# Kernel tuning notes

Hardware: AMD Instinct MI355X
Metric: run time of the kernel (lower is better)

## Reference

```python
import jax, jax.numpy as jnp
import numpy as np

B, C, H, W = 64, 3, 64, 64
F = 96          # base_filters
K = 8           # n_mixtures
h, w = H // 2, W // 2
C0 = 2 * C      # channels of each checkerboard half
SECTIONS = [C0, C0, C0 * K, C0 * K, C0 * K]
SPLITS = [int(s) for s in np.cumsum(SECTIONS)[:-1]]
EPS = 1e-6


def conv2d(x, wgt, b):
    y = jax.lax.conv_general_dilated(x, wgt, (1, 1), 'SAME',
                                     dimension_numbers=('NCHW', 'OIHW', 'NCHW'))
    return y + b[None, :, None, None]


def layer_norm(x, g, b, eps=1e-5):
    # nn.LayerNorm(mid_shape): normalize over (C,H,W) per sample
    mu = jnp.mean(x, axis=(1, 2, 3), keepdims=True)
    var = jnp.var(x, axis=(1, 2, 3), keepdims=True)
    return (x - mu) / jnp.sqrt(var + eps) * g[None] + b[None]


def checker_split(z, odd=False):
    Bz, Cz, Hz, Wz = z.shape
    z = z.reshape(Bz, Cz, Hz // 2, 2, Wz // 2, 2)
    p00 = z[:, :, :, 0, :, 0]; p01 = z[:, :, :, 0, :, 1]
    p10 = z[:, :, :, 1, :, 0]; p11 = z[:, :, :, 1, :, 1]
    z0 = jnp.concatenate([p00, p11], axis=1)  # even checkerboard
    z1 = jnp.concatenate([p01, p10], axis=1)  # odd checkerboard
    if odd:
        z0, z1 = z1, z0
    return z0, z1


def checker_merge(z0, z1, odd=False):
    if odd:
        z0, z1 = z1, z0
    Cz = z0.shape[1] // 2
    p00, p11 = z0[:, :Cz], z0[:, Cz:]
    p01, p10 = z1[:, :Cz], z1[:, Cz:]
    Bz, _, hz, wz = p00.shape
    zi = jnp.stack([jnp.stack([p00, p01], axis=-1),
                    jnp.stack([p10, p11], axis=-1)], axis=-2)  # (B,C,h,w,2i,2j)
    z = zi.transpose(0, 1, 2, 4, 3, 5).reshape(Bz, Cz, 2 * hz, 2 * wz)
    return z


def gated_attn(x, qkv_w, qkv_b, proj_w, proj_b):
    Bx, Fx, hx, wx = x.shape
    xf = x.reshape(Bx, Fx, hx * wx).transpose(0, 2, 1)  # (B, L, F)
    qkv = xf @ qkv_w.T + qkv_b
    q, k, v = jnp.split(qkv, 3, axis=-1)
    scores = jnp.einsum('bqf,bkf->bqk', q, k) / jnp.sqrt(jnp.float32(Fx))
    attn = jax.nn.softmax(scores, axis=-1)
    o = jnp.einsum('bqk,bkf->bqf', attn, v)
    g = o @ proj_w.T + proj_b
    ga, gb = jnp.split(g, 2, axis=-1)
    out = xf + ga * jax.nn.sigmoid(gb)  # gated residual
    return out.transpose(0, 2, 1).reshape(Bx, Fx, hx, wx)


def conditioner(z1, conv1_w, conv1_b, gconv_w, gconv_b, ln1_g, ln1_b,
                qkv_w, qkv_b, proj_w, proj_b, ln2_g, ln2_b, conv2_w, conv2_b):
    x = conv2d(z1, conv1_w, conv1_b)
    g = conv2d(x, gconv_w, gconv_b)
    ga, gb = jnp.split(g, 2, axis=1)
    x = x + ga * jax.nn.sigmoid(gb)          # GatedConv2d
    x = layer_norm(x, ln1_g, ln1_b)
    x = gated_attn(x, qkv_w, qkv_b, proj_w, proj_b)
    x = layer_norm(x, ln2_g, ln2_b)
    return conv2d(x, conv2_w, conv2_b)


def _forward(z, log_df_dz, conv1_w, conv1_b, gconv_w, gconv_b, ln1_g, ln1_b,
             qkv_w, qkv_b, proj_w, proj_b, ln2_g, ln2_b, conv2_w, conv2_b,
             a_log_scale, a_bias):
    z0, z1 = checker_split(z)
    params = conditioner(z1, conv1_w, conv1_b, gconv_w, gconv_b, ln1_g, ln1_b,
                         qkv_w, qkv_b, proj_w, proj_b, ln2_g, ln2_b, conv2_w, conv2_b)
    a, b, logpi, mu, s = jnp.split(params, SPLITS, axis=1)
    a = jnp.tanh(a) * a_log_scale + a_bias
    Bz = z0.shape[0]
    logpi = jax.nn.log_softmax(logpi.reshape(Bz, K, C0, h, w), axis=1)
    mu = mu.reshape(Bz, K, C0, h, w)
    s = s.reshape(Bz, K, C0, h, w)
    # mixture-of-logistics CDF
    u = (z0[:, None] - mu) * jnp.exp(-s)
    x = jnp.sum(jnp.exp(logpi) * jax.nn.sigmoid(u), axis=1)
    log_pdf = jax.scipy.special.logsumexp(
        logpi - s + jax.nn.log_sigmoid(u) + jax.nn.log_sigmoid(-u), axis=1)
    log_df_dz = log_df_dz + jnp.sum(log_pdf.reshape(Bz, -1), axis=1)
    # logit transform
    x = jnp.clip(x, EPS, 1.0 - EPS)
    z0n = jnp.log(x) - jnp.log1p(-x)
    log_df_dz = log_df_dz + jnp.sum((-jnp.log(x) - jnp.log1p(-x)).reshape(Bz, -1), axis=1)
    # affine rescale
    z0n = z0n * jnp.exp(a) + b
    log_df_dz = log_df_dz + jnp.sum(a.reshape(Bz, -1), axis=1)
    return checker_merge(z0n, z1), log_df_dz


def setup_inputs() -> dict:
    key = jax.random.key(0)
    ks = jax.random.split(key, 10)
    sc = 0.05
    return dict(
        z=jax.random.normal(ks[0], (B, C, H, W), jnp.float32),
        log_df_dz=jnp.zeros((B,), jnp.float32),
        conv1_w=sc * jax.random.normal(ks[1], (F, C0, 3, 3), jnp.float32),
        conv1_b=jnp.zeros((F,), jnp.float32),
        gconv_w=sc * jax.random.normal(ks[2], (2 * F, F, 3, 3), jnp.float32),
        gconv_b=jnp.zeros((2 * F,), jnp.float32),
        ln1_g=jnp.ones((F, h, w), jnp.float32),
        ln1_b=jnp.zeros((F, h, w), jnp.float32),
        qkv_w=sc * jax.random.normal(ks[3], (3 * F, F), jnp.float32),
        qkv_b=jnp.zeros((3 * F,), jnp.float32),
        proj_w=sc * jax.random.normal(ks[4], (2 * F, F), jnp.float32),
        proj_b=jnp.zeros((2 * F,), jnp.float32),
        ln2_g=jnp.ones((F, h, w), jnp.float32),
        ln2_b=jnp.zeros((F, h, w), jnp.float32),
        conv2_w=sc * jax.random.normal(ks[5], (sum(SECTIONS), F, 3, 3), jnp.float32),
        conv2_b=jnp.zeros((sum(SECTIONS),), jnp.float32),
        a_log_scale=0.01 * jax.random.normal(ks[6], (1,), jnp.float32),
        a_bias=0.01 * jax.random.normal(ks[7], (1,), jnp.float32),
    )


def reference(z, log_df_dz, conv1_w, conv1_b, gconv_w, gconv_b, ln1_g, ln1_b,
              qkv_w, qkv_b, proj_w, proj_b, ln2_g, ln2_b, conv2_w, conv2_b,
              a_log_scale, a_bias):
    return _forward(z, log_df_dz, conv1_w, conv1_b, gconv_w, gconv_b, ln1_g, ln1_b,
                    qkv_w, qkv_b, proj_w, proj_b, ln2_g, ln2_b, conv2_w, conv2_b,
                    a_log_scale, a_bias)
```

## Files before the change

### kernel.cpp

```cpp
#include <hip/hip_runtime.h>
#include <cstdint>
#include <cstddef>


typedef unsigned short u16;
typedef __attribute__((ext_vector_type(8))) short short8;
typedef __attribute__((ext_vector_type(4))) float f32x4;
typedef __attribute__((ext_vector_type(4))) unsigned int u32x4;

__device__ __forceinline__ float sigm(float x){ return 1.0f/(1.0f+__expf(-x)); }

__device__ __forceinline__ u16 f2bf(float f){
    unsigned int u = __float_as_uint(f);
    u += 0x7fffu + ((u >> 16) & 1u);
    return (u16)(u >> 16);
}
__device__ __forceinline__ float bf2f(u16 v){
    unsigned int u = ((unsigned int)v) << 16;
    return __uint_as_float(u);
}

__device__ __forceinline__ void dma16(const u16* g, u16* l){
    __builtin_amdgcn_global_load_lds(
        (const __attribute__((address_space(1))) void*)g,
        (__attribute__((address_space(3))) void*)l,
        16, 0, 0);
}

__device__ __forceinline__ float ex2(float x){
    float r; asm("v_exp_f32 %0, %1" : "=v"(r) : "v"(x)); return r;
}
__device__ __forceinline__ unsigned cvtpk(float lo, float hi){
    unsigned r; asm("v_cvt_pk_bf16_f32 %0, %1, %2" : "=v"(r) : "v"(lo), "v"(hi)); return r;
}
__device__ __forceinline__ void plswap32(unsigned &a, unsigned &b){
    asm("v_permlane32_swap_b32 %0, %1" : "+v"(a), "+v"(b));
}
__device__ __forceinline__ void plswap16(unsigned &a, unsigned &b){
    asm("v_permlane16_swap_b32 %0, %1" : "+v"(a), "+v"(b));
}

#define SOFTPACK(S, LACC, PA) do { \
    unsigned pk_[4][2]; \
    _Pragma("unroll") \
    for (int t=0;t<4;++t){ \
        float e0 = ex2(S[t][0]); \
        float e1 = ex2(S[t][1]); \
        float e2 = ex2(S[t][2]); \
        float e3 = ex2(S[t][3]); \
        LACC += (e0+e1)+(e2+e3); \
        pk_[t][0] = cvtpk(e0,e1); \
        pk_[t][1] = cvtpk(e2,e3); \
    } \
    _Pragma("unroll") \
    for (int kk=0;kk<2;++kk){ \
        unsigned a0 = pk_[2*kk][0], b0 = pk_[2*kk+1][0]; \
        unsigned a1 = pk_[2*kk][1], b1 = pk_[2*kk+1][1]; \
        plswap32(a0,b0); plswap16(a0,b0); \
        plswap32(a1,b1); plswap16(a1,b1); \
        u32x4 dw_; dw_[0]=a0; dw_[1]=a1; dw_[2]=b0; dw_[3]=b1; \
        PA[kk] = __builtin_bit_cast(short8, dw_); \
    } \
} while(0)

__device__ __forceinline__ short8 ln_frag(const u16* __restrict__ xg,
    const float* __restrict__ gt, const float* __restrict__ bt,
    int p, int c0, float mu, float rr)
{
    short8 x8 = *reinterpret_cast<const short8*>(xg + (size_t)p*96 + c0);
    const float* gp = gt + (size_t)p*96 + c0;
    const float* bp = bt + (size_t)p*96 + c0;
    short8 o;
    #pragma unroll
    for (int j=0;j<8;++j){
        float ag = rr*gp[j];
        o[j] = (short)f2bf(bf2f((u16)x8[j])*ag + (bp[j] - mu*ag));
    }
    return o;
}

__global__ __launch_bounds__(256) void k_prep(
    const float* __restrict__ z, const float* __restrict__ c1w, const float* __restrict__ c1b,
    const float* __restrict__ gw, const float* __restrict__ c2w,
    const float* __restrict__ qkvw, const float* __restrict__ pw,
    const float* __restrict__ ln1g, const float* __restrict__ ln1b,
    const float* __restrict__ ln2g, const float* __restrict__ ln2b,
    const float* __restrict__ logdf,
    u16* __restrict__ x1b,
    u16* __restrict__ Wg, u16* __restrict__ W2,
    u16* __restrict__ Wqkv, u16* __restrict__ Wproj,
    float* __restrict__ gt1, float* __restrict__ bt1,
    float* __restrict__ gt2, float* __restrict__ bt2,
    float* __restrict__ outlog)
{
    int blk = blockIdx.x;
    int tid = threadIdx.x;
    __shared__ float tin[6][6][34];
    __shared__ __align__(16) u16 Wc[96][72];
    __shared__ __align__(16) u16 imc[128][72];

    if (blk < 512){
        int b  = blk >> 3;
        int pg = blk & 7;
        int r0 = pg*4;
        for (int e = tid; e < 96*72; e += 256){
            int oc = e/72, k = e%72;
            Wc[oc][k] = (k < 54) ? f2bf(c1w[oc*54 + k]) : (u16)0;
        }
        for (int idx = tid; idx < 6*6*34; idx += 256){
            int c = idx/204, rem = idx%204;
            int rr = rem/34, q = rem%34;
            int ii = r0 - 1 + rr, jj = q - 1;
            float v = 0.f;
            if ((unsigned)ii < 32u && (unsigned)jj < 32u){
                if (c < 3) v = z[((b*3+c)*64 + 2*ii)*64 + (2*jj+1)];
                else       v = z[((b*3+(c-3))*64 + (2*ii+1))*64 + 2*jj];
            }
            tin[c][rr][q] = v;
        }
        __syncthreads();
        for (int e = tid; e < 128*72; e += 256){
            int px = e/72, k = e%72;
            float v = 0.f;
            if (k < 54){
                int c = k/9, rr = (k%9)/3, dcc = k%3;
                v = tin[c][(px>>5)+rr][(px&31)+dcc];
            }
            imc[px][k] = f2bf(v);
        }
        __syncthreads();

        int w = tid >> 6, lane = tid & 63;
        int cc = lane & 15, gg = lane >> 4;
        f32x4 acc[2][6];
        #pragma unroll
        for (int u=0;u<2;++u)
            #pragma unroll
            for (int t=0;t<6;++t) acc[u][t] = (f32x4){0.f,0.f,0.f,0.f};

        #pragma unroll
        for (int ks=0; ks<2; ++ks){
            short8 a0 = *reinterpret_cast<const short8*>(&imc[w*32 + cc     ][ks*32 + 8*gg]);
            short8 a1 = *reinterpret_cast<const short8*>(&imc[w*32 + 16 + cc][ks*32 + 8*gg]);
            #pragma unroll
            for (int t=0; t<6; ++t){
                short8 bb = *reinterpret_cast<const short8*>(&Wc[t*16+cc][ks*32 + 8*gg]);
                acc[0][t] = __builtin_amdgcn_mfma_f32_16x16x32_bf16(a0, bb, acc[0][t], 0,0,0);
                acc[1][t] = __builtin_amdgcn_mfma_f32_16x16x32_bf16(a1, bb, acc[1][t], 0,0,0);
            }
        }

        #pragma unroll
        for (int u=0;u<2;++u){
            int p0 = pg*128 + w*32 + u*16 + gg*4;
            #pragma unroll
            for (int t=0;t<6;++t){
                int oc = t*16+cc;
                float bv = c1b[oc];
                #pragma unroll
                for (int r=0;r<4;++r)
                    x1b[((size_t)(b*1024) + p0 + r)*96 + oc] = f2bf(acc[u][t][r] + bv);
            }
        }
    } else if (blk < 1160){
        int idx = (blk-512)*256 + tid;
        int j = idx & 7;
        int lane = (idx >> 3) & 63;
        int fo = idx >> 9;
        int frag = fo % 18;
        int tob = fo / 18;
        int obk = tob & 1, tap = tob >> 1;
        int t = frag/3, ks = frag%3;
        int cc = lane & 15, gg = lane >> 4;
        int ocp = obk*96 + t*16 + cc;
        int r2 = ocp%96, isB = r2/48, i2 = r2%48;
        int oc = (ocp/96)*48 + i2 + isB*96;
        int ic = ks*32 + 8*gg + j;
        Wg[idx] = f2bf(gw[(size_t)(oc*96+ic)*9 + tap]);
    } else if (blk < 1700){
        int idx = (blk-1160)*256 + tid;
        int j = idx & 7;
        int lane = (idx >> 3) & 63;
        int fo = idx >> 9;
        int frag = fo % 15;
        int tob = fo / 15;
        int obk = tob & 1, tap = tob >> 1;
        int t = frag/3, ks = frag%3;
        int cc = lane & 15, gg = lane >> 4;
        int oc = obk*80 + t*16 + cc;
        int ic = ks*32 + 8*gg + j;
        W2[idx] = (oc < 156) ? f2bf(c2w[(size_t)(oc*96+ic)*9 + tap]) : (u16)0;
    } else if (blk < 1808){
        int idx = (blk-1700)*256 + tid;
        int j = idx & 7;
        int lane = (idx >> 3) & 63;
        int fo = idx >> 9;
        int frag = fo % 27;
        int obk = fo / 27;
        int t = frag/3, ks = frag%3;
        int cc = lane & 15, gg = lane >> 4;
        int n = obk*144 + t*16 + cc;
        int ic = ks*32 + 8*gg + j;
        Wqkv[idx] = f2bf(qkvw[(size_t)n*96 + ic]);
    } else if (blk < 1880){
        int idx = (blk-1808)*256 + tid;
        int j = idx & 7;
        int lane = (idx >> 3) & 63;
        int fo = idx >> 9;
        int frag = fo % 18;
        int obk = fo / 18;
        int t = frag/3, ks = frag%3;
        int cc = lane & 15, gg = lane >> 4;
        int ocp = obk*96 + t*16 + cc;
        int r2 = ocp%96, isB = r2/48, i2 = r2%48;
        int oc = obk*48 + i2 + isB*96;
        int ic = ks*32 + 8*gg + j;
        Wproj[idx] = f2bf(pw[(size_t)oc*96 + ic]);
    } else if (blk < 2264){
        int idx = (blk-1880)*256 + tid;
        int c = idx >> 10, p = idx & 1023;
        gt1[p*96 + c] = ln1g[idx];
    } else if (blk < 2648){
        int idx = (blk-2264)*256 + tid;
        int c = idx >> 10, p = idx & 1023;
        bt1[p*96 + c] = ln1b[idx];
    } else if (blk < 3032){
        int idx = (blk-2648)*256 + tid;
        int c = idx >> 10, p = idx & 1023;
        gt2[p*96 + c] = ln2g[idx];
    } else if (blk < 3416){
        int idx = (blk-3032)*256 + tid;
        int c = idx >> 10, p = idx & 1023;
        bt2[p*96 + c] = ln2b[idx];
    } else {
        if (tid < 64) outlog[tid] = logdf[tid];
    }
}

__global__ __launch_bounds__(256,4) void k_gconv(const u16* __restrict__ Xpb,
    const u16* __restrict__ Wt, const float* __restrict__ bias,
    u16* __restrict__ outb, float* __restrict__ partials)
{
    int blk  = blockIdx.x;
    int obk  = blk & 1;
    int pblk = (blk >> 1) & 7;
    int b    = blk >> 4;
    int tid  = threadIdx.x;
    int w = tid >> 6, lane = tid & 63;
    int cc = lane & 15, gg = lane >> 4;

    __shared__ __align__(16) u16 Ws[2][9216];
    __shared__ float red[8];

    f32x4 acc[2][6];
    #pragma unroll
    for (int u=0;u<2;++u)
        #pragma unroll
        for (int t=0;t<6;++t) acc[u][t] = (f32x4){0.f,0.f,0.f,0.f};

    int base = pblk*128 + w*32;
    int ia = base >> 5;
    const u16* xb = Xpb + (size_t)b*1024*96;

    {
        const u16* src = Wt + (size_t)obk*9216;
        #pragma unroll
        for (int i=0;i<5;++i){
            int c = tid + 256*i;
            if (c < 1152) dma16(src + (size_t)c*8, Ws[0] + (size_t)(w*64+256*i)*8);
        }
    }

    for (int tap=0; tap<9; ++tap){
        __syncthreads();
        if (tap < 8){
            const u16* src = Wt + (size_t)((tap+1)*2 + obk)*9216;
            int nb = (tap+1)&1;
            #pragma unroll
            for (int i=0;i<5;++i){
                int c = tid + 256*i;
                if (c < 1152) dma16(src + (size_t)c*8, Ws[nb] + (size_t)(w*64+256*i)*8);
            }
        }
        const u16* Wc = Ws[tap&1];
        int dr = tap/3 - 1, dc = tap%3 - 1;

        int ii = ia + dr;
        int jj0 = cc + dc, jj1 = cc + 16 + dc;
        bool rv = ((unsigned)ii < 32u);
        bool v0 = rv && ((unsigned)jj0 < 32u);
        bool v1 = rv && ((unsigned)jj1 < 32u);
        const u16* ar0 = xb + (ptrdiff_t)(ii*32 + jj0)*96 + 8*gg;
        const u16* ar1 = xb + (ptrdiff_t)(ii*32 + jj1)*96 + 8*gg;

        #pragma unroll
        for (int ks=0; ks<3; ++ks){
            short8 a0 = {0,0,0,0,0,0,0,0};
            short8 a1 = {0,0,0,0,0,0,0,0};
            if (v0) a0 = *reinterpret_cast<const short8*>(ar0 + ks*32);
            if (v1) a1 = *reinterpret_cast<const short8*>(ar1 + ks*32);
            #pragma unroll
            for (int t=0; t<6; ++t){
                short8 bb = *reinterpret_cast<const short8*>(Wc + ((size_t)(t*3+ks)*64 + lane)*8);
                acc[0][t] = __builtin_amdgcn_mfma_f32_16x16x32_bf16(a0, bb, acc[0][t], 0,0,0);
                acc[1][t] = __builtin_amdgcn_mfma_f32_16x16x32_bf16(a1, bb, acc[1][t], 0,0,0);
            }
        }
    }

    float s = 0.f, ssq = 0.f;
    #pragma unroll
    for (int u=0;u<2;++u){
        int p0 = base + u*16 + gg*4;
        #pragma unroll
        for (int t=0;t<3;++t){
            int ocA = obk*48 + t*16+cc;
            float ba = bias[ocA], bbv = bias[ocA+96];
            #pragma unroll
            for (int r=0;r<4;++r){
                float res = bf2f(Xpb[((size_t)b*1024 + p0+r)*96 + ocA]);
                float va = acc[u][t][r]   + ba;
                float vb = acc[u][t+3][r] + bbv;
                float v = res + va*sigm(vb);
                outb[((size_t)b*1024 + p0+r)*96 + ocA] = f2bf(v);
                s += v; ssq += v*v;
            }
        }
    }
    #pragma unroll
    for (int o=32;o>0;o>>=1){ s += __shfl_down(s,o,64); ssq += __shfl_down(ssq,o,64); }
    if (lane==0){ red[w]=s; red[4+w]=ssq; }
    __syncthreads();
    if (tid==0){
        int slot = b*16 + pblk*2 + obk;
        partials[slot*2+0] = red[0]+red[1]+red[2]+red[3];
        partials[slot*2+1] = red[4]+red[5]+red[6]+red[7];
    }
}

__global__ __launch_bounds__(256) void k_lne(const u16* __restrict__ xb,
    const float* __restrict__ gt, const float* __restrict__ bt,
    const float* __restrict__ partials, u16* __restrict__ out)
{
    int b = blockIdx.x / 48, rem = blockIdx.x % 48;
    float s=0.f, ss=0.f;
    #pragma unroll
    for (int i=0;i<16;++i){ s += partials[(b*16+i)*2]; ss += partials[(b*16+i)*2+1]; }
    float mu = s/98304.f;
    float r = rsqrtf(ss/98304.f - mu*mu + 1e-5f);

    int e8 = rem*256 + threadIdx.x;
    size_t base = (size_t)b*98304 + (size_t)e8*8;
    short8 x8 = *reinterpret_cast<const short8*>(xb + base);
    const float* gp = gt + e8*8;
    const float* bp = bt + e8*8;
    short8 o8;
    #pragma unroll
    for (int i=0;i<8;++i)
        o8[i] = (short)f2bf((bf2f((u16)x8[i]) - mu)*r*gp[i] + bp[i]);
    *reinterpret_cast<short8*>(out + base) = o8;
}

__global__ __launch_bounds__(256,4) void k_conv2m(const u16* __restrict__ Xpb,
    const u16* __restrict__ Wt, const float* __restrict__ bias,
    u16* __restrict__ out)
{
    int blk  = blockIdx.x;
    int obk  = blk & 1;
    int pblk = (blk >> 1) & 7;
    int b    = blk >> 4;
    int tid  = threadIdx.x;
    int w = tid >> 6, lane = tid & 63;
    int cc = lane & 15, gg = lane >> 4;

    __shared__ __align__(16) u16 Ws[2][7680];

    f32x4 acc[2][5];
    #pragma unroll
    for (int u=0;u<2;++u)
        #pragma unroll
        for (int t=0;t<5;++t) acc[u][t] = (f32x4){0.f,0.f,0.f,0.f};

    int base = pblk*128 + w*32;
    int ia = base >> 5;
    const u16* xb = Xpb + (size_t)b*1024*96;

    {
        const u16* src = Wt + (size_t)obk*7680;
        #pragma unroll
        for (int i=0;i<4;++i){
            int c = tid + 256*i;
            if (c < 960) dma16(src + (size_t)c*8, Ws[0] + (size_t)(w*64+256*i)*8);
        }
    }

    for (int tap=0; tap<9; ++tap){
        __syncthreads();
        if (tap < 8){
            const u16* src = Wt + (size_t)((tap+1)*2 + obk)*7680;
            int nb = (tap+1)&1;
            #pragma unroll
            for (int i=0;i<4;++i){
                int c = tid + 256*i;
                if (c < 960) dma16(src + (size_t)c*8, Ws[nb] + (size_t)(w*64+256*i)*8);
            }
        }
        const u16* Wc = Ws[tap&1];
        int dr = tap/3 - 1, dc = tap%3 - 1;

        int ii = ia + dr;
        int jj0 = cc + dc, jj1 = cc + 16 + dc;
        bool rv = ((unsigned)ii < 32u);
        bool v0 = rv && ((unsigned)jj0 < 32u);
        bool v1 = rv && ((unsigned)jj1 < 32u);
        const u16* ar0 = xb + (ptrdiff_t)(ii*32 + jj0)*96 + 8*gg;
        const u16* ar1 = xb + (ptrdiff_t)(ii*32 + jj1)*96 + 8*gg;

        #pragma unroll
        for (int ks=0; ks<3; ++ks){
            short8 a0 = {0,0,0,0,0,0,0,0};
            short8 a1 = {0,0,0,0,0,0,0,0};
            if (v0) a0 = *reinterpret_cast<const short8*>(ar0 + ks*32);
            if (v1) a1 = *reinterpret_cast<const short8*>(ar1 + ks*32);
            #pragma unroll
            for (int t=0; t<5; ++t){
                short8 bb = *reinterpret_cast<const short8*>(Wc + ((size_t)(t*3+ks)*64 + lane)*8);
                acc[0][t] = __builtin_amdgcn_mfma_f32_16x16x32_bf16(a0, bb, acc[0][t], 0,0,0);
                acc[1][t] = __builtin_amdgcn_mfma_f32_16x16x32_bf16(a1, bb, acc[1][t], 0,0,0);
            }
        }
    }

    #pragma unroll
    for (int u=0;u<2;++u){
        int p0 = base + u*16 + gg*4;
        #pragma unroll
        for (int t=0;t<5;++t){
            int oc = obk*80 + t*16+cc;
            if (oc < 156){
                float bv = bias[oc];
                u16* op = out + ((size_t)b*156 + oc)*1024 + p0;
                #pragma unroll
                for (int r=0;r<4;++r) op[r] = f2bf(acc[u][t][r] + bv);
            }
        }
    }
}

__global__ __launch_bounds__(256,4) void k_qkvm(const u16* __restrict__ Xg,
    const float* __restrict__ gt, const float* __restrict__ bt,
    const float* __restrict__ part,
    const u16* __restrict__ Wt, const float* __restrict__ bias,
    u16* __restrict__ Qb, u16* __restrict__ Kf, u16* __restrict__ Vf)
{
    int blk  = blockIdx.x;
    int obk  = blk & 1;
    int pblk = (blk >> 1) & 7;
    int b    = blk >> 4;
    int tid  = threadIdx.x;
    int w = tid >> 6, lane = tid & 63;
    int cc = lane & 15, gg = lane >> 4;
    const float scale = 0.14724445f;

    __shared__ __align__(16) u16 Ws[13824];
    {
        const u16* src = Wt + (size_t)obk*13824;
        #pragma unroll
        for (int i=0;i<7;++i){
            int c = tid + 256*i;
            if (c < 1728) dma16(src + (size_t)c*8, Ws + (size_t)(w*64+256*i)*8);
        }
    }

    float sS=0.f, sQ=0.f;
    #pragma unroll
    for (int i=0;i<16;++i){ sS += part[(b*16+i)*2]; sQ += part[(b*16+i)*2+1]; }
    float mu = sS/98304.f;
    float rr = rsqrtf(sQ/98304.f - mu*mu + 1e-5f);

    f32x4 acc[2][9];
    #pragma unroll
    for (int u=0;u<2;++u)
        #pragma unroll
        for (int t=0;t<9;++t) acc[u][t] = (f32x4){0.f,0.f,0.f,0.f};

    int base = pblk*128 + w*32;
    const u16* xg = Xg + (size_t)b*1024*96;
    __syncthreads();

    #pragma unroll
    for (int ks=0; ks<3; ++ks){
        int c0 = ks*32 + 8*gg;
        short8 a0 = ln_frag(xg, gt, bt, base+cc,    c0, mu, rr);
        short8 a1 = ln_frag(xg, gt, bt, base+cc+16, c0, mu, rr);
        #pragma unroll
        for (int t=0; t<9; ++t){
            short8 bb = *reinterpret_cast<const short8*>(Ws + ((size_t)(t*3+ks)*64 + lane)*8);
            acc[0][t] = __builtin_amdgcn_mfma_f32_16x16x32_bf16(a0, bb, acc[0][t], 0,0,0);
            acc[1][t] = __builtin_amdgcn_mfma_f32_16x16x32_bf16(a1, bb, acc[1][t], 0,0,0);
        }
    }

    #pragma unroll
    for (int u=0;u<2;++u){
        int p0 = base + u*16 + gg*4;
        #pragma unroll
        for (int t=0;t<9;++t){
            int n = obk*144 + t*16+cc;
            float bv = bias[n];
            #pragma unroll
            for (int r=0;r<4;++r){
                int p = p0 + r;
                float av = acc[u][t][r] + bv;
                if (n < 96){
                    Qb[((size_t)(b*1024+p))*96 + n] = f2bf(av*scale);
                } else if (n < 192){
                    int f = n-96;
                    int jt = p>>6, t16 = (p>>4)&3, ccs = p&15;
                    int ks = f>>5, ggs = (f>>3)&3, j = f&7;
                    Kf[(size_t)(b*16+jt)*6144 + (size_t)(((t16*3+ks)*4+ggs)*16+ccs)*8 + j] = f2bf(av);
                } else {
                    int f = n-192;
                    int jt = p>>6, kl = p&63;
                    int kk = kl>>5, ggs = (kl>>3)&3, j = kl&7;
                    int ft = f>>4, ccs = f&15;
                    Vf[(size_t)(b*16+jt)*6144 + (size_t)(((ft*2+kk)*4+ggs)*16+ccs)*8 + j] = f2bf(av);
                }
            }
        }
    }
}

__global__ __launch_bounds__(256,2) void k_attn(const u16* __restrict__ Qb,
    const u16* __restrict__ Kf, const u16* __restrict__ Vf, u16* __restrict__ Ob)
{
    int qt = blockIdx.x >> 6;
    int b  = blockIdx.x & 63;
    int tid = threadIdx.x;
    int w  = tid >> 6;
    int lane = tid & 63;
    int cc = lane & 15;
    int gg = lane >> 4;

    __shared__ __align__(16) u16 Ks[3][6144];
    __shared__ __align__(16) u16 Vs[3][6144];

    int q0 = qt*128 + w*32;

    short8 qf[2][3];
    {
        const u16* qr0 = Qb + ((size_t)(b*1024 + q0 + cc))*96;
        #pragma unroll
        for (int ks=0; ks<3; ++ks){
            qf[0][ks] = *reinterpret_cast<const short8*>(qr0 + ks*32 + 8*gg);
            qf[1][ks] = *reinterpret_cast<const short8*>(qr0 + (size_t)16*96 + ks*32 + 8*gg);
        }
    }

    f32x4 Oacc[2][6];
    #pragma unroll
    for (int u=0;u<2;++u)
        #pragma unroll
        for (int ft=0; ft<6; ++ft) Oacc[u][ft] = (f32x4){0.f,0.f,0.f,0.f};
    float l_acc[2] = {0.f, 0.f};

    const u16* Kb0 = Kf + (size_t)(b*16)*6144;
    const u16* Vb0 = Vf + (size_t)(b*16)*6144;

    #pragma unroll
    for (int i=0;i<3;++i){
        size_t c8 = (size_t)(tid + 256*i)*8;
        size_t l8 = (size_t)(w*64 + 256*i)*8;
        dma16(Kb0 + c8, Ks[0] + l8);
        dma16(Vb0 + c8, Vs[0] + l8);
    }
    #pragma unroll
    for (int i=0;i<3;++i){
        size_t c8 = (size_t)(6144 + (tid + 256*i)*8);
        size_t l8 = (size_t)(w*64 + 256*i)*8;
        dma16(Kb0 + c8, Ks[1] + l8);
        dma16(Vb0 + c8, Vs[1] + l8);
    }

    for (int jt=0; jt<16; ++jt){
        if (jt < 15) asm volatile("s_waitcnt vmcnt(6)" ::: "memory");
        else         asm volatile("s_waitcnt vmcnt(0)" ::: "memory");
        __builtin_amdgcn_s_barrier();
        __builtin_amdgcn_sched_barrier(0);

        if (jt < 14){
            const u16* kn = Kb0 + (size_t)(jt+2)*6144;
            const u16* vn = Vb0 + (size_t)(jt+2)*6144;
            u16* kd = Ks[(jt+2)%3];
            u16* vd = Vs[(jt+2)%3];
            #pragma unroll
            for (int i=0;i<3;++i){
                size_t c8 = (size_t)(tid + 256*i)*8;
                size_t l8 = (size_t)(w*64 + 256*i)*8;
                dma16(kn + c8, kd + l8);
                dma16(vn + c8, vd + l8);
            }
        }

        const u16* Kc = Ks[jt%3];
        const u16* Vc = Vs[jt%3];

        f32x4 S0[4], S1[4];
        #pragma unroll
        for (int t=0;t<4;++t){ S0[t] = (f32x4){0.f,0.f,0.f,0.f}; S1[t] = (f32x4){0.f,0.f,0.f,0.f}; }

        __builtin_amdgcn_s_setprio(1);
        #pragma unroll
        for (int ks=0; ks<3; ++ks){
            #pragma unroll
            for (int t=0; t<4; ++t){
                short8 kb = *reinterpret_cast<const short8*>(Kc + ((t*3+ks)*64 + lane)*8);
                S0[t] = __builtin_amdgcn_mfma_f32_16x16x32_bf16(kb, qf[0][ks], S0[t], 0,0,0);
                S1[t] = __builtin_amdgcn_mfma_f32_16x16x32_bf16(kb, qf[1][ks], S1[t], 0,0,0);
            }
        }
        __builtin_amdgcn_s_setprio(0);

        short8 pa0[2], pa1[2];
        SOFTPACK(S0, l_acc[0], pa0);
        SOFTPACK(S1, l_acc[1], pa1);

        __builtin_amdgcn_s_setprio(1);
        #pragma unroll
        for (int kk=0; kk<2; ++kk){
            #pragma unroll
            for (int ft=0; ft<6; ++ft){
                short8 vb = *reinterpret_cast<const short8*>(Vc + ((ft*2+kk)*64 + lane)*8);
                Oacc[0][ft] = __builtin_amdgcn_mfma_f32_16x16x32_bf16(pa0[kk], vb, Oacc[0][ft], 0,0,0);
                Oacc[1][ft] = __builtin_amdgcn_mfma_f32_16x16x32_bf16(pa1[kk], vb, Oacc[1][ft], 0,0,0);
            }
        }
        __builtin_amdgcn_s_setprio(0);
    }

    #pragma unroll
    for (int u=0;u<2;++u){
        float lv = l_acc[u];
        lv += __shfl_xor(lv, 16, 64);
        lv += __shfl_xor(lv, 32, 64);
        float linv[4];
        #pragma unroll
        for (int r=0;r<4;++r) linv[r] = 1.0f / __shfl(lv, 4*gg + r, 64);
        #pragma unroll
        for (int ft=0; ft<6; ++ft)
            #pragma unroll
            for (int r=0; r<4; ++r)
                Ob[((size_t)(b*1024 + q0 + u*16 + 4*gg + r))*96 + ft*16 + cc]
                    = f2bf(Oacc[u][ft][r]*linv[r]);
    }
}

__global__ __launch_bounds__(256,4) void k_projm(const u16* __restrict__ Opb,
    const u16* __restrict__ Wt, const float* __restrict__ bias,
    const u16* __restrict__ Xg, const float* __restrict__ gt, const float* __restrict__ bt,
    const float* __restrict__ part1,
    u16* __restrict__ outb, float* __restrict__ partials)
{
    int blk  = blockIdx.x;
    int obk  = blk & 1;
    int pblk = (blk >> 1) & 7;
    int b    = blk >> 4;
    int tid  = threadIdx.x;
    int w = tid >> 6, lane = tid & 63;
    int cc = lane & 15, gg = lane >> 4;

    __shared__ __align__(16) u16 Ws[9216];
    __shared__ float red[8];
    {
        const u16* src = Wt + (size_t)obk*9216;
        #pragma unroll
        for (int i=0;i<5;++i){
            int c = tid + 256*i;
            if (c < 1152) dma16(src + (size_t)c*8, Ws + (size_t)(w*64+256*i)*8);
        }
    }

    float sS=0.f, sQ=0.f;
    #pragma unroll
    for (int i=0;i<16;++i){ sS += part1[(b*16+i)*2]; sQ += part1[(b*16+i)*2+1]; }
    float mu1 = sS/98304.f;
    float rr1 = rsqrtf(sQ/98304.f - mu1*mu1 + 1e-5f);

    f32x4 acc[2][6];
    #pragma unroll
    for (int u=0;u<2;++u)
        #pragma unroll
        for (int t=0;t<6;++t) acc[u][t] = (f32x4){0.f,0.f,0.f,0.f};

    int base = pblk*128 + w*32;
    const u16* xb = Opb + ((size_t)b*1024 + base)*96;
    __syncthreads();

    #pragma unroll
    for (int ks=0; ks<3; ++ks){
        short8 a0 = *reinterpret_cast<const short8*>(xb + (size_t)cc*96      + ks*32 + 8*gg);
        short8 a1 = *reinterpret_cast<const short8*>(xb + (size_t)(cc+16)*96 + ks*32 + 8*gg);
        #pragma unroll
        for (int t=0; t<6; ++t){
            short8 bb = *reinterpret_cast<const short8*>(Ws + ((size_t)(t*3+ks)*64 + lane)*8);
            acc[0][t] = __builtin_amdgcn_mfma_f32_16x16x32_bf16(a0, bb, acc[0][t], 0,0,0);
            acc[1][t] = __builtin_amdgcn_mfma_f32_16x16x32_bf16(a1, bb, acc[1][t], 0,0,0);
        }
    }

    const u16* resb = Xg + (size_t)b*1024*96;
    float s = 0.f, ssq = 0.f;
    #pragma unroll
    for (int u=0;u<2;++u){
        int p0 = base + u*16 + gg*4;
        #pragma unroll
        for (int t=0;t<3;++t){
            int ocA = obk*48 + t*16+cc;
            float ba = bias[ocA], bbv = bias[ocA+96];
            #pragma unroll
            for (int r=0;r<4;++r){
                int pl = p0 + r;
                float ga = acc[u][t][r]   + ba;
                float gb = acc[u][t+3][r] + bbv;
                float xv = bf2f(resb[(size_t)pl*96 + ocA]);
                float res = (xv - mu1)*rr1*gt[(size_t)pl*96 + ocA] + bt[(size_t)pl*96 + ocA];
                float v = res + ga * sigm(gb);
                outb[((size_t)b*1024 + pl)*96 + ocA] = f2bf(v);
                s += v; ssq += v*v;
            }
        }
    }
    #pragma unroll
    for (int o=32;o>0;o>>=1){ s += __shfl_down(s,o,64); ssq += __shfl_down(ssq,o,64); }
    if (lane==0){ red[w]=s; red[4+w]=ssq; }
    __syncthreads();
    if (tid==0){
        int slot = b*16 + pblk*2 + obk;
        partials[slot*2+0] = red[0]+red[1]+red[2]+red[3];
        partials[slot*2+1] = red[4]+red[5]+red[6]+red[7];
    }
}

__global__ __launch_bounds__(256) void k_mix(const float* __restrict__ z,
    const u16* __restrict__ params, const float* __restrict__ a_ls_p,
    const float* __restrict__ a_b_p, float* __restrict__ out_z, float* __restrict__ out_log)
{
    int b = blockIdx.x / 24;
    int rem = blockIdx.x % 24;
    int c0 = rem / 4;
    int pix = (rem & 3)*256 + threadIdx.x;
    int i = pix >> 5, j = pix & 31;
    float als = a_ls_p[0], abv = a_b_p[0];
    const u16* pb = params + (size_t)b*156*1024;
    float logacc = 0.f;

    if (c0 < 3){
        int idx01 = ((b*3+c0)*64 + 2*i)*64 + 2*j+1;
        int idx10 = ((b*3+c0)*64 + 2*i+1)*64 + 2*j;
        out_z[idx01] = z[idx01];
        out_z[idx10] = z[idx10];
    }

    {
        float z0v = (c0<3) ? z[((b*3+c0)*64 + 2*i)*64 + 2*j]
                           : z[((b*3+(c0-3))*64 + 2*i+1)*64 + 2*j+1];
        float a_raw = bf2f(pb[(c0)*1024 + pix]);
        float bco   = bf2f(pb[(6+c0)*1024 + pix]);
        float lp[8], mu[8], sv[8];
        float m1 = -1e30f;
        #pragma unroll
        for (int k=0;k<8;++k){
            lp[k] = bf2f(pb[(12 + k*6 + c0)*1024 + pix]);
            mu[k] = bf2f(pb[(60 + k*6 + c0)*1024 + pix]);
            sv[k] = bf2f(pb[(108 + k*6 + c0)*1024 + pix]);
            m1 = fmaxf(m1, lp[k]);
        }
        float se = 0.f;
        #pragma unroll
        for (int k=0;k<8;++k) se += __expf(lp[k]-m1);
        float lse = m1 + __logf(se);
        float xm = 0.f, mt = -1e30f;
        float t[8];
        #pragma unroll
        for (int k=0;k<8;++k){
            float lpn = lp[k] - lse;
            float u = (z0v - mu[k]) * __expf(-sv[k]);
            float au = fabsf(u);
            xm += __expf(lpn) * (1.f/(1.f+__expf(-u)));
            float lss = -(au + 2.f*log1pf(__expf(-au)));
            float tk = lpn - sv[k] + lss;
            t[k] = tk; mt = fmaxf(mt, tk);
        }
        float se2 = 0.f;
        #pragma unroll
        for (int k=0;k<8;++k) se2 += __expf(t[k]-mt);
        logacc += mt + __logf(se2);
        xm = fminf(fmaxf(xm, 1e-6f), 1.f-1e-6f);
        float lx = __logf(xm), l1x = log1pf(-xm);
        logacc += -lx - l1x;
        float aa = tanhf(a_raw)*als + abv;
        float z0n = (lx - l1x)*__expf(aa) + bco;
        logacc += aa;
        int oidx = (c0<3) ? ((b*3+c0)*64 + 2*i)*64 + 2*j
                          : ((b*3+(c0-3))*64 + 2*i+1)*64 + 2*j+1;
        out_z[oidx] = z0n;
    }

    #pragma unroll
    for (int o=32;o>0;o>>=1) logacc += __shfl_down(logacc, o, 64);
    __shared__ float part[4];
    if ((threadIdx.x&63)==0) part[threadIdx.x>>6] = logacc;
    __syncthreads();
    if (threadIdx.x==0){
        atomicAdd(out_log + b, part[0]+part[1]+part[2]+part[3]);
    }
}

extern "C" void kernel_launch(void* const* d_in, const int* in_sizes, int n_in,
                              void* d_out, int out_size, void* d_ws, size_t ws_size,
                              hipStream_t stream)
{
    const float* z     = (const float*)d_in[0];
    const float* logdf = (const float*)d_in[1];
    const float* c1w   = (const float*)d_in[2];
    const float* c1b   = (const float*)d_in[3];
    const float* gw    = (const float*)d_in[4];
    const float* gcb   = (const float*)d_in[5];
    const float* ln1g  = (const float*)d_in[6];
    const float* ln1b  = (const float*)d_in[7];
    const float* qkvw  = (const float*)d_in[8];
    const float* qkvb  = (const float*)d_in[9];
    const float* pw    = (const float*)d_in[10];
    const float* pbb   = (const float*)d_in[11];
    const float* ln2g  = (const float*)d_in[12];
    const float* ln2b  = (const float*)d_in[13];
    const float* c2w   = (const float*)d_in[14];
    const float* c2b   = (const float*)d_in[15];
    const float* als   = (const float*)d_in[16];
    const float* ab    = (const float*)d_in[17];

    float* out_z   = (float*)d_out;
    float* out_log = out_z + 786432;

    float* ws     = (float*)d_ws;
    u16*   x1b    = (u16*)(ws + 0);
    u16*   xg_b   = (u16*)(ws + 3145728);
    u16*   Kf     = (u16*)(ws + 6291456);
    u16*   Vf     = (u16*)(ws + 9437184);
    u16*   Ob     = (u16*)(ws + 12582912);
    u16*   x2b    = (u16*)(ws + 15728640);
    u16*   Qb     = x1b;
    u16*   xln2b  = Kf;
    u16*   params = (u16*)(ws + 9437184);
    const size_t T = 19660800;
    float* gt1    = ws + T;
    float* bt1    = ws + T + 98304;
    float* gt2    = ws + T + 196608;
    float* bt2    = ws + T + 294912;
    float* part1  = ws + T + 393216;
    float* part2  = ws + T + 395264;
    u16*   Wg     = (u16*)(ws + T + 397568);
    u16*   W2     = (u16*)(ws + T + 480512);
    u16*   Wqkv   = (u16*)(ws + T + 549632);
    u16*   Wproj  = (u16*)(ws + T + 563456);

    k_prep   <<<3417, 256, 0, stream>>>(z, c1w, c1b, gw, c2w, qkvw, pw,
                                        ln1g, ln1b, ln2g, ln2b, logdf,
                                        x1b, Wg, W2, Wqkv, Wproj,
                                        gt1, bt1, gt2, bt2, out_log);
    k_gconv  <<<1024, 256, 0, stream>>>(x1b, Wg, gcb, xg_b, part1);
    k_qkvm   <<<1024, 256, 0, stream>>>(xg_b, gt1, bt1, part1, Wqkv, qkvb, Qb, Kf, Vf);
    k_attn   <<<512, 256, 0, stream>>>(Qb, Kf, Vf, Ob);
    k_projm  <<<1024, 256, 0, stream>>>(Ob, Wproj, pbb, xg_b, gt1, bt1, part1, x2b, part2);
    k_lne    <<<3072, 256, 0, stream>>>(x2b, gt2, bt2, part2, xln2b);
    k_conv2m <<<1024, 256, 0, stream>>>(xln2b, W2, c2b, params);
    k_mix    <<<1536, 256, 0, stream>>>(z, params, als, ab, out_z, out_log);
}
```

Before: 269.8 us.

## Fuse conv2 and mixture-logistic coupling into one kernel via shared memory

Merges the final 3x3 conv (k_conv2m) and the mixture coupling kernel (k_mix) into one kernel. Each block now computes all 156 output channels for its 128-pixel tile, stages the bf16 params in LDS and runs the mixture math directly from LDS. This removes the global write and read of the params tensor and one launch. In exchange each block does twice the MFMA work with twice as many accumulators, uses about 60KB of LDS, and launches only 512 blocks at an occupancy bound of 2, which lowers parallelism.

```diff
diff --git a/kernel.cpp b/kernel.cpp
--- a/kernel.cpp
+++ b/kernel.cpp
@@ -361,92 +361,6 @@
     *reinterpret_cast<short8*>(out + base) = o8;
 }
 
-__global__ __launch_bounds__(256,4) void k_conv2m(const u16* __restrict__ Xpb,
-    const u16* __restrict__ Wt, const float* __restrict__ bias,
-    u16* __restrict__ out)
-{
-    int blk  = blockIdx.x;
-    int obk  = blk & 1;
-    int pblk = (blk >> 1) & 7;
-    int b    = blk >> 4;
-    int tid  = threadIdx.x;
-    int w = tid >> 6, lane = tid & 63;
-    int cc = lane & 15, gg = lane >> 4;
-
-    __shared__ __align__(16) u16 Ws[2][7680];
-
-    f32x4 acc[2][5];
-    #pragma unroll
-    for (int u=0;u<2;++u)
-        #pragma unroll
-        for (int t=0;t<5;++t) acc[u][t] = (f32x4){0.f,0.f,0.f,0.f};
-
-    int base = pblk*128 + w*32;
-    int ia = base >> 5;
-    const u16* xb = Xpb + (size_t)b*1024*96;
-
-    {
-        const u16* src = Wt + (size_t)obk*7680;
-        #pragma unroll
-        for (int i=0;i<4;++i){
-            int c = tid + 256*i;
-            if (c < 960) dma16(src + (size_t)c*8, Ws[0] + (size_t)(w*64+256*i)*8);
-        }
-    }
-
-    for (int tap=0; tap<9; ++tap){
-        __syncthreads();
-        if (tap < 8){
-            const u16* src = Wt + (size_t)((tap+1)*2 + obk)*7680;
-            int nb = (tap+1)&1;
-            #pragma unroll
-            for (int i=0;i<4;++i){
-                int c = tid + 256*i;
-                if (c < 960) dma16(src + (size_t)c*8, Ws[nb] + (size_t)(w*64+256*i)*8);
-            }
-        }
-        const u16* Wc = Ws[tap&1];
-        int dr = tap/3 - 1, dc = tap%3 - 1;
-
-        int ii = ia + dr;
-        int jj0 = cc + dc, jj1 = cc + 16 + dc;
-        bool rv = ((unsigned)ii < 32u);
-        bool v0 = rv && ((unsigned)jj0 < 32u);
-        bool v1 = rv && ((unsigned)jj1 < 32u);
-        const u16* ar0 = xb + (ptrdiff_t)(ii*32 + jj0)*96 + 8*gg;
-        const u16* ar1 = xb + (ptrdiff_t)(ii*32 + jj1)*96 + 8*gg;
-
-        #pragma unroll
-        for (int ks=0; ks<3; ++ks){
-            short8 a0 = {0,0,0,0,0,0,0,0};
-            short8 a1 = {0,0,0,0,0,0,0,0};
-            if (v0) a0 = *reinterpret_cast<const short8*>(ar0 + ks*32);
-            if (v1) a1 = *reinterpret_cast<const short8*>(ar1 + ks*32);
-            #pragma unroll
-            for (int t=0; t<5; ++t){
-                short8 bb = *reinterpret_cast<const short8*>(Wc + ((size_t)(t*3+ks)*64 + lane)*8);
-                acc[0][t] = __builtin_amdgcn_mfma_f32_16x16x32_bf16(a0, bb, acc[0][t], 0,0,0);
-                acc[1][t] = __builtin_amdgcn_mfma_f32_16x16x32_bf16(a1, bb, acc[1][t], 0,0,0);
-            }
-        }
-    }
-
-    #pragma unroll
-    for (int u=0;u<2;++u){
-        int p0 = base + u*16 + gg*4;
-        #pragma unroll
-        for (int t=0;t<5;++t){
-            int oc = obk*80 + t*16+cc;
-            if (oc < 156){
-                float bv = bias[oc];
-                u16* op = out + ((size_t)b*156 + oc)*1024 + p0;
-                #pragma unroll
-                for (int r=0;r<4;++r) op[r] = f2bf(acc[u][t][r] + bv);
-            }
-        }
-    }
-}
-
 __global__ __launch_bounds__(256,4) void k_qkvm(const u16* __restrict__ Xg,
     const float* __restrict__ gt, const float* __restrict__ bt,
     const float* __restrict__ part,
@@ -741,60 +655,143 @@
     }
 }
 
-__global__ __launch_bounds__(256) void k_mix(const float* __restrict__ z,
-    const u16* __restrict__ params, const float* __restrict__ a_ls_p,
+__global__ __launch_bounds__(256,2) void k_c2mix(const u16* __restrict__ Xpb,
+    const u16* __restrict__ Wt, const float* __restrict__ bias,
+    const float* __restrict__ z, const float* __restrict__ a_ls_p,
     const float* __restrict__ a_b_p, float* __restrict__ out_z, float* __restrict__ out_log)
 {
-    int b = blockIdx.x / 24;
-    int rem = blockIdx.x % 24;
-    int c0 = rem / 4;
-    int pix = (rem & 3)*256 + threadIdx.x;
-    int i = pix >> 5, j = pix & 31;
+    int blk  = blockIdx.x;
+    int pblk = blk & 7;
+    int b    = blk >> 3;
+    int tid  = threadIdx.x;
+    int w = tid >> 6, lane = tid & 63;
+    int cc = lane & 15, gg = lane >> 4;
+
+    __shared__ __align__(16) u16 SM[30720];
+    __shared__ float red[4];
+
+    f32x4 acc[2][10];
+    #pragma unroll
+    for (int u=0;u<2;++u)
+        #pragma unroll
+        for (int t=0;t<10;++t) acc[u][t] = (f32x4){0.f,0.f,0.f,0.f};
+
+    int base = pblk*128 + w*32;
+    int ia = base >> 5;
+    const u16* xb = Xpb + (size_t)b*1024*96;
+
+    {
+        #pragma unroll
+        for (int i=0;i<8;++i){
+            int c = tid + 256*i;
+            if (c < 1920) dma16(Wt + (size_t)c*8, SM + (size_t)(w*64+256*i)*8);
+        }
+    }
+
+    for (int tap=0; tap<9; ++tap){
+        __syncthreads();
+        if (tap < 8){
+            const u16* src = Wt + (size_t)(tap+1)*15360;
+            u16* dst = SM + (size_t)((tap+1)&1)*15360;
+            #pragma unroll
+            for (int i=0;i<8;++i){
+                int c = tid + 256*i;
+                if (c < 1920) dma16(src + (size_t)c*8, dst + (size_t)(w*64+256*i)*8);
+            }
+        }
+        const u16* Wc = SM + (size_t)(tap&1)*15360;
+        int dr = tap/3 - 1, dc = tap%3 - 1;
+
+        int ii = ia + dr;
+        int jj0 = cc + dc, jj1 = cc + 16 + dc;
+        bool rv = ((unsigned)ii < 32u);
+        bool v0 = rv && ((unsigned)jj0 < 32u);
+        bool v1 = rv && ((unsigned)jj1 < 32u);
+        const u16* ar0 = xb + (ptrdiff_t)(ii*32 + jj0)*96 + 8*gg;
+        const u16* ar1 = xb + (ptrdiff_t)(ii*32 + jj1)*96 + 8*gg;
+
+        #pragma unroll
+        for (int ks=0; ks<3; ++ks){
+            short8 a0 = {0,0,0,0,0,0,0,0};
+            short8 a1 = {0,0,0,0,0,0,0,0};
+            if (v0) a0 = *reinterpret_cast<const short8*>(ar0 + ks*32);
+            if (v1) a1 = *reinterpret_cast<const short8*>(ar1 + ks*32);
+            #pragma unroll
+            for (int t=0; t<10; ++t){
+                int fl = (t<5) ? (t*3+ks) : (15 + (t-5)*3 + ks);
+                short8 bb = *reinterpret_cast<const short8*>(Wc + ((size_t)fl*64 + lane)*8);
+                acc[0][t] = __builtin_amdgcn_mfma_f32_16x16x32_bf16(a0, bb, acc[0][t], 0,0,0);
+                acc[1][t] = __builtin_amdgcn_mfma_f32_16x16x32_bf16(a1, bb, acc[1][t], 0,0,0);
+            }
+        }
+    }
+
+    __syncthreads();
+    #pragma unroll
+    for (int u=0;u<2;++u){
+        int lp0 = w*32 + u*16 + gg*4;
+        #pragma unroll
+        for (int t=0;t<10;++t){
+            int oc = (t<5) ? (t*16+cc) : (80 + (t-5)*16 + cc);
+            if (oc < 156){
+                float bv = bias[oc];
+                #pragma unroll
+                for (int r=0;r<4;++r)
+                    SM[oc*132 + lp0 + r] = f2bf(acc[u][t][r] + bv);
+            }
+        }
+    }
+    __syncthreads();
+
     float als = a_ls_p[0], abv = a_b_p[0];
-    const u16* pb = params + (size_t)b*156*1024;
-    float logacc = 0.f;
-
-    if (c0 < 3){
-        int idx01 = ((b*3+c0)*64 + 2*i)*64 + 2*j+1;
-        int idx10 = ((b*3+c0)*64 + 2*i+1)*64 + 2*j;
-        out_z[idx01] = z[idx01];
-        out_z[idx10] = z[idx10];
-    }
-
-    {
+    float logsum = 0.f;
+    #pragma unroll
+    for (int e3=0;e3<3;++e3){
+        int e  = tid + 256*e3;
+        int c0 = e >> 7, xp = e & 127;
+        int pix = pblk*128 + xp;
+        int i = pix >> 5, j = pix & 31;
+
+        if (c0 < 3){
+            int idx01 = ((b*3+c0)*64 + 2*i)*64 + 2*j+1;
+            int idx10 = ((b*3+c0)*64 + 2*i+1)*64 + 2*j;
+            out_z[idx01] = z[idx01];
+            out_z[idx10] = z[idx10];
+        }
+
         float z0v = (c0<3) ? z[((b*3+c0)*64 + 2*i)*64 + 2*j]
                            : z[((b*3+(c0-3))*64 + 2*i+1)*64 + 2*j+1];
-        float a_raw = bf2f(pb[(c0)*1024 + pix]);
-        float bco   = bf2f(pb[(6+c0)*1024 + pix]);
-        float lp[8], mu[8], sv[8];
+        float a_raw = bf2f(SM[(c0)*132 + xp]);
+        float bco   = bf2f(SM[(6+c0)*132 + xp]);
+        float lpk[8], muk[8], svk[8];
         float m1 = -1e30f;
         #pragma unroll
         for (int k=0;k<8;++k){
-            lp[k] = bf2f(pb[(12 + k*6 + c0)*1024 + pix]);
-            mu[k] = bf2f(pb[(60 + k*6 + c0)*1024 + pix]);
-            sv[k] = bf2f(pb[(108 + k*6 + c0)*1024 + pix]);
-            m1 = fmaxf(m1, lp[k]);
+            lpk[k] = bf2f(SM[(12 + k*6 + c0)*132 + xp]);
+            muk[k] = bf2f(SM[(60 + k*6 + c0)*132 + xp]);
+            svk[k] = bf2f(SM[(108 + k*6 + c0)*132 + xp]);
+            m1 = fmaxf(m1, lpk[k]);
         }
         float se = 0.f;
         #pragma unroll
-        for (int k=0;k<8;++k) se += __expf(lp[k]-m1);
+        for (int k=0;k<8;++k) se += __expf(lpk[k]-m1);
         float lse = m1 + __logf(se);
         float xm = 0.f, mt = -1e30f;
-        float t[8];
+        float tk[8];
         #pragma unroll
         for (int k=0;k<8;++k){
-            float lpn = lp[k] - lse;
-            float u = (z0v - mu[k]) * __expf(-sv[k]);
+            float lpn = lpk[k] - lse;
+            float u = (z0v - muk[k]) * __expf(-svk[k]);
             float au = fabsf(u);
             xm += __expf(lpn) * (1.f/(1.f+__expf(-u)));
             float lss = -(au + 2.f*log1pf(__expf(-au)));
-            float tk = lpn - sv[k] + lss;
-            t[k] = tk; mt = fmaxf(mt, tk);
+            float t2 = lpn - svk[k] + lss;
+            tk[k] = t2; mt = fmaxf(mt, t2);
         }
         float se2 = 0.f;
         #pragma unroll
-        for (int k=0;k<8;++k) se2 += __expf(t[k]-mt);
-        logacc += mt + __logf(se2);
+        for (int k=0;k<8;++k) se2 += __expf(tk[k]-mt);
+        float logacc = mt + __logf(se2);
         xm = fminf(fmaxf(xm, 1e-6f), 1.f-1e-6f);
         float lx = __logf(xm), l1x = log1pf(-xm);
         logacc += -lx - l1x;
@@ -804,16 +801,14 @@
         int oidx = (c0<3) ? ((b*3+c0)*64 + 2*i)*64 + 2*j
                           : ((b*3+(c0-3))*64 + 2*i+1)*64 + 2*j+1;
         out_z[oidx] = z0n;
-    }
-
-    #pragma unroll
-    for (int o=32;o>0;o>>=1) logacc += __shfl_down(logacc, o, 64);
-    __shared__ float part[4];
-    if ((threadIdx.x&63)==0) part[threadIdx.x>>6] = logacc;
+        logsum += logacc;
+    }
+
+    #pragma unroll
+    for (int o=32;o>0;o>>=1) logsum += __shfl_down(logsum, o, 64);
+    if (lane==0) red[w] = logsum;
     __syncthreads();
-    if (threadIdx.x==0){
-        atomicAdd(out_log + b, part[0]+part[1]+part[2]+part[3]);
-    }
+    if (tid==0) atomicAdd(out_log + b, red[0]+red[1]+red[2]+red[3]);
 }
 
 extern "C" void kernel_launch(void* const* d_in, const int* in_sizes, int n_in,
@@ -851,7 +846,6 @@
     u16*   x2b    = (u16*)(ws + 15728640);
     u16*   Qb     = x1b;
     u16*   xln2b  = Kf;
-    u16*   params = (u16*)(ws + 9437184);
     const size_t T = 19660800;
     float* gt1    = ws + T;
     float* bt1    = ws + T + 98304;
@@ -873,6 +867,5 @@
     k_attn   <<<512, 256, 0, stream>>>(Qb, Kf, Vf, Ob);
     k_projm  <<<1024, 256, 0, stream>>>(Ob, Wproj, pbb, xg_b, gt1, bt1, part1, x2b, part2);
     k_lne    <<<3072, 256, 0, stream>>>(x2b, gt2, bt2, part2, xln2b);
-    k_conv2m <<<1024, 256, 0, stream>>>(xln2b, W2, c2b, params);
-    k_mix    <<<1536, 256, 0, stream>>>(z, params, als, ab, out_z, out_log);
-}
+    k_c2mix  <<<512,  256, 0, stream>>>(xln2b, W2, c2b, z, als, ab, out_z, out_log);
+}
```

After: 256.2 us. 5.1% less time.
